# Kernel tuning notes

Measured on AMD Instinct MI355X. Metric: run time of the kernel, lower is better.

## Reference

```python
import jax, jax.numpy as jnp
import numpy as np

B, INPUTDIM, OUTDIM, GRIDSIZE = 4096, 128, 512, 300

def setup_inputs() -> dict:
    key = jax.random.key(0)
    k1, k2 = jax.random.split(key)
    x = jax.random.normal(k1, (B, INPUTDIM), dtype=jnp.float32)
    scale = 1.0 / (np.sqrt(INPUTDIM) * np.sqrt(GRIDSIZE))
    fouriercoeffs = jax.random.normal(k2, (2, OUTDIM, INPUTDIM, GRIDSIZE), dtype=jnp.float32) * scale
    return {"x": x, "fouriercoeffs": fouriercoeffs}

def reference(x, fouriercoeffs):
    # k: frequencies 1..gridsize
    gridsize = fouriercoeffs.shape[-1]
    k = jnp.arange(1, gridsize + 1, dtype=x.dtype)  # (G,)
    arg = x[:, :, None] * k  # (B, I, G)
    c = jnp.cos(arg)
    s = jnp.sin(arg)
    # einsum('dbik,djik->bj') with d=2 split into cos/sin terms
    y = jnp.einsum('big,jig->bj', c, fouriercoeffs[0]) + jnp.einsum('big,jig->bj', s, fouriercoeffs[1])
    return y
```

## Files before the change

### kernel.cpp

```cpp
#include <hip/hip_runtime.h>
#include <hip/hip_bf16.h>
#include <cstdint>

#define TB 256

typedef short short8 __attribute__((ext_vector_type(8)));
typedef float f32x4 __attribute__((ext_vector_type(4)));

constexpr int B_N = 4096, I_N = 128, J_N = 512, G_N = 300;
constexpr int K1 = I_N * G_N;
constexpr int BM = 128, BN = 256;
constexpr int NSP = 8;
constexpr int IC = 16;
constexpr float INV2PI = 0.15915494309189535f;

constexpr int GSTRIDE = 4 * 512 * 8;
constexpr size_t SPSTRIDE = (size_t)G_N * GSTRIDE;

__device__ __forceinline__ ushort f2bf(float f) {
    unsigned int u = __float_as_uint(f);
    return (ushort)((u + 0x7FFFu + ((u >> 16) & 1u)) >> 16);
}

__device__ __forceinline__ float fract_(float x) {
#if __has_builtin(__builtin_amdgcn_fractf)
    return __builtin_amdgcn_fractf(x);
#else
    return x - floorf(x);
#endif
}

__device__ __forceinline__ unsigned int pack_bf2(float a, float b) {
    __hip_bfloat162 h = __float22bfloat162_rn(make_float2(a, b));
    unsigned int u;
    __builtin_memcpy(&u, &h, 4);
    return u;
}

typedef __attribute__((address_space(3))) unsigned int lds_u32_t;
typedef __attribute__((address_space(1))) const unsigned int glb_u32_t;

__device__ __forceinline__ void llds16(const void* g, void* l) {
    __builtin_amdgcn_global_load_lds(
        reinterpret_cast<glb_u32_t*>(reinterpret_cast<uintptr_t>(g)),
        reinterpret_cast<lds_u32_t*>((unsigned int)reinterpret_cast<uintptr_t>(l)),
        16, 0, 0);
}

constexpr int TGC = 12;
__global__ __launch_bounds__(TB) void fkan_tr(const float* __restrict__ src,
                                              ushort* __restrict__ dst) {
    __shared__ __align__(16) ushort L[TGC * 2 * 32 * 8];
    const int bx = blockIdx.x;
    const int sp = bx & 7, djc = (bx >> 3) & 31, gc = bx >> 8;
    const int dj0 = djc * 32;
    const int d = dj0 >> 9;
    const int j0 = dj0 & 511;
    const int g0 = gc * TGC;
    const int tid = threadIdx.x;
    const int djl = tid >> 3, i2 = tid & 7;
    const int iA = sp * 16 + i2 * 2;
    const size_t rowA = ((size_t)(dj0 + djl) * 128 + iA) * 300;
    const int ihl = i2 >> 2;
    const int eA = (i2 & 3) * 2;

#pragma unroll
    for (int gq = 0; gq < TGC / 4; ++gq) {
        const int gg = g0 + gq * 4;
        float4 va = *(const float4*)(src + rowA + gg);
        float4 vb = *(const float4*)(src + rowA + 300 + gg);
        float a[4] = {va.x, va.y, va.z, va.w};
        float b[4] = {vb.x, vb.y, vb.z, vb.w};
#pragma unroll
        for (int t = 0; t < 4; ++t) {
            int gl = gq * 4 + t;
            unsigned int w = (unsigned int)f2bf(a[t]) | ((unsigned int)f2bf(b[t]) << 16);
            *(unsigned int*)&L[(((gl * 2 + ihl) * 32 + djl) * 8 + eA)] = w;
        }
    }
    __syncthreads();
    const uint4* Lv = (const uint4*)L;
#pragma unroll
    for (int it = 0; it < 3; ++it) {
        int s = it * 256 + tid;
        int gl = s >> 6, r = s & 63;
        int ih = r >> 5, jl = r & 31;
        size_t d16 = ((size_t)(sp * G_N + g0 + gl) * 4 + d * 2 + ih) * 512 + j0 + jl;
        ((uint4*)dst)[d16] = Lv[s];
    }
}

__global__ __launch_bounds__(TB, 2)
void fkan_gemm(const float* __restrict__ x,
               const ushort* __restrict__ fcb,
               float* __restrict__ out) {
    __shared__ __align__(16) ushort At[2 * 4 * 128 * 8];
    __shared__ __align__(16) ushort Bt[2 * 4 * 256 * 8];

    const int tid = threadIdx.x;
    const int bm = blockIdx.x, bn = blockIdx.y, sp = blockIdx.z;
    const int lane = tid & 63, wid = tid >> 6;
    const int wm = wid & 1, wn = wid >> 1;
    const int lhi = lane >> 4, llo = lane & 15;
    const int m = tid & 127, half = tid >> 7;

    float sv[8], cv[8], s0[8], c0[8];
    {
        const float* xr = x + ((size_t)(bm * BM + m)) * I_N + sp * IC + half * 8;
        float4 xa = *(const float4*)xr;
        float4 xb = *(const float4*)(xr + 4);
        float xv[8] = {xa.x, xa.y, xa.z, xa.w, xb.x, xb.y, xb.z, xb.w};
#pragma unroll
        for (int j = 0; j < 8; ++j) {
            float r = fract_(xv[j] * INV2PI);
            s0[j] = __builtin_amdgcn_sinf(r);
            c0[j] = __builtin_amdgcn_cosf(r);
            sv[j] = s0[j];
            cv[j] = c0[j];
        }
    }

    const ushort* bp[4];
#pragma unroll
    for (int q = 0; q < 4; ++q)
        bp[q] = fcb + (size_t)sp * SPSTRIDE
              + ((size_t)wid * 512 + bn * BN + q * 64 + lane) * 8;

    const int aoff = (lhi * 128 + wm * 64 + llo) * 8;
    const int boff = (lhi * 256 + wn * 128 + llo) * 8;
    ushort* awc0 = &At[(half * 128 + m) * 8];
    ushort* aws0 = &At[((2 + half) * 128 + m) * 8];

    f32x4 acc[4][8];
#pragma unroll
    for (int a = 0; a < 4; ++a)
#pragma unroll
        for (int b = 0; b < 8; ++b) acc[a][b] = (f32x4){0.f, 0.f, 0.f, 0.f};

    auto stageB = [&](int nb) {
#pragma unroll
        for (int q = 0; q < 4; ++q) {
            llds16(bp[q], (char*)Bt + (size_t)(nb * 1024 + wid * 256 + q * 64) * 16);
            bp[q] += GSTRIDE;
        }
    };
    auto writeA = [&](int nb) {
        uint4 vc = {pack_bf2(cv[0], cv[1]), pack_bf2(cv[2], cv[3]),
                    pack_bf2(cv[4], cv[5]), pack_bf2(cv[6], cv[7])};
        *(uint4*)(awc0 + nb * 4096) = vc;
        uint4 vs = {pack_bf2(sv[0], sv[1]), pack_bf2(sv[2], sv[3]),
                    pack_bf2(sv[4], sv[5]), pack_bf2(sv[6], sv[7])};
        *(uint4*)(aws0 + nb * 4096) = vs;
#pragma unroll
        for (int j = 0; j < 8; ++j) {
            float t = __builtin_fmaf(sv[j], c0[j], cv[j] * s0[j]);
            cv[j] = __builtin_fmaf(cv[j], c0[j], -(sv[j] * s0[j]));
            sv[j] = t;
        }
    };
    auto halfstep = [&](int cb, bool doNext) {
        __syncthreads();
        short8 af[4], bfr[8];
#pragma unroll
        for (int t = 0; t < 4; ++t)
            af[t] = *(const short8*)&At[cb * 4096 + aoff + t * 128];
#pragma unroll
        for (int t = 0; t < 8; ++t)
            bfr[t] = *(const short8*)&Bt[cb * 8192 + boff + t * 128];
        if (doNext) stageB(cb ^ 1);
#pragma unroll
        for (int tm = 0; tm < 4; ++tm)
#pragma unroll
            for (int tn = 0; tn < 8; ++tn)
                acc[tm][tn] = __builtin_amdgcn_mfma_f32_16x16x32_bf16(
                    af[tm], bfr[tn], acc[tm][tn], 0, 0, 0);
        if (doNext) writeA(cb ^ 1);
    };

    writeA(0);
    stageB(0);

    for (int g = 0; g < G_N; g += 2) {
        halfstep(0, true);
        halfstep(1, g + 2 < G_N);
    }

    const int row0 = bm * BM + wm * 64 + lhi * 4;
    const int col0 = bn * BN + wn * 128 + llo;
#pragma unroll
    for (int tm = 0; tm < 4; ++tm)
#pragma unroll
        for (int tn = 0; tn < 8; ++tn)
#pragma unroll
            for (int r = 0; r < 4; ++r)
                atomicAdd(&out[(size_t)(row0 + tm * 16 + r) * J_N + col0 + tn * 16],
                          acc[tm][tn][r]);
}

constexpr int SPL_FB = 4;
constexpr int KS_FB = 2 * K1 / SPL_FB;
constexpr int NSTEP_FB = KS_FB / 32;

__global__ __launch_bounds__(TB)
void fkan_gemm_fb(const float* __restrict__ x,
                  const float* __restrict__ fc32,
                  float* __restrict__ out) {
    __shared__ float xs[BM][65];
    __shared__ __align__(16) ushort At[4 * 128 * 8];
    __shared__ __align__(16) ushort Bt[4 * 128 * 8];

    const int tid = threadIdx.x;
    const int bm = blockIdx.x, bn = blockIdx.y, sp = blockIdx.z;
    const int d = sp >> 1;
    const int ib = (sp & 1) << 6;
    const int rbase = ib * G_N;

    for (int idx = tid; idx < BM * 64; idx += TB) {
        int row = idx >> 6, il = idx & 63;
        xs[row][il] = x[(size_t)(bm * BM + row) * I_N + ib + il];
    }

    f32x4 acc[4][4];
#pragma unroll
    for (int a = 0; a < 4; ++a)
#pragma unroll
        for (int b = 0; b < 4; ++b) acc[a][b] = (f32x4){0.f, 0.f, 0.f, 0.f};

    const int lane = tid & 63, wid = tid >> 6;
    const int wm = wid & 1, wn = wid >> 1;
    const int lhi = lane >> 4, llo = lane & 15;
    const int am = tid & 127, akg0 = tid >> 7;

    const float* f32base = fc32 + ((size_t)d * J_N + bn * 128) * K1 + rbase;

    for (int step = 0; step < NSTEP_FB; ++step) {
        __syncthreads();
#pragma unroll
        for (int it = 0; it < 2; ++it) {
            const int kg = akg0 + it * 2;
            int r = rbase + step * 32 + kg * 8;
            int i = (int)((unsigned)r / 300u);
            int g = r - i * 300;
            float xxv = xs[am][i - ib];
            float kkf = (float)(g + 1);
            short8 avv;
#pragma unroll
            for (int j = 0; j < 8; ++j) {
                float rev = xxv * kkf * INV2PI;
                float fr = fract_(rev) + (d ? 0.0f : 0.25f);
                avv[j] = (short)f2bf(__builtin_amdgcn_sinf(fract_(fr)));
                if (j < 7) {
                    ++g; kkf += 1.0f;
                    if (g == 300) { g = 0; kkf = 1.0f; ++i; xxv = xs[am][i - ib]; }
                }
            }
            *(short8*)&At[(kg * 128 + am) * 8] = avv;
        }
#pragma unroll
        for (int it = 0; it < 2; ++it) {
            int item = tid + it * TB;
            int n = item >> 2, grp = item & 3;
            const float* gp = f32base + (size_t)n * K1 + step * 32 + grp * 8;
            float4 v0 = *(const float4*)gp;
            float4 v1 = *(const float4*)(gp + 4);
            short8 bv;
            bv[0] = (short)f2bf(v0.x); bv[1] = (short)f2bf(v0.y);
            bv[2] = (short)f2bf(v0.z); bv[3] = (short)f2bf(v0.w);
            bv[4] = (short)f2bf(v1.x); bv[5] = (short)f2bf(v1.y);
            bv[6] = (short)f2bf(v1.z); bv[7] = (short)f2bf(v1.w);
            *(short8*)&Bt[(grp * 128 + n) * 8] = bv;
        }
        __syncthreads();
        short8 af[4], bf[4];
#pragma unroll
        for (int t = 0; t < 4; ++t) {
            af[t] = *(const short8*)&At[(lhi * 128 + wm * 64 + t * 16 + llo) * 8];
            bf[t] = *(const short8*)&Bt[(lhi * 128 + wn * 64 + t * 16 + llo) * 8];
        }
#pragma unroll
        for (int tm = 0; tm < 4; ++tm)
#pragma unroll
            for (int tn = 0; tn < 4; ++tn)
                acc[tm][tn] = __builtin_amdgcn_mfma_f32_16x16x32_bf16(
                    af[tm], bf[tn], acc[tm][tn], 0, 0, 0);
    }

    const int row0 = bm * BM + wm * 64 + lhi * 4;
    const int col0 = bn * 128 + wn * 64 + llo;
#pragma unroll
    for (int tm = 0; tm < 4; ++tm)
#pragma unroll
        for (int tn = 0; tn < 4; ++tn)
#pragma unroll
            for (int r = 0; r < 4; ++r)
                atomicAdd(&out[(size_t)(row0 + tm * 16 + r) * J_N + col0 + tn * 16],
                          acc[tm][tn][r]);
}

extern "C" void kernel_launch(void* const* d_in, const int* in_sizes, int n_in,
                              void* d_out, int out_size, void* d_ws, size_t ws_size,
                              hipStream_t stream) {
    const float* x = (const float*)d_in[0];
    const float* fc = (const float*)d_in[1];
    float* out = (float*)d_out;

    hipMemsetAsync(d_out, 0, (size_t)out_size * sizeof(float), stream);

    const size_t need = (size_t)2 * J_N * K1 * sizeof(ushort);

    if (ws_size >= need) {
        ushort* fcb = (ushort*)d_ws;
        fkan_tr<<<25 * 32 * 8, TB, 0, stream>>>(fc, fcb);
        dim3 grid(B_N / BM, J_N / BN, NSP);
        fkan_gemm<<<grid, TB, 0, stream>>>(x, fcb, out);
    } else {
        dim3 grid(B_N / BM, J_N / 128, SPL_FB);
        fkan_gemm_fb<<<grid, TB, 0, stream>>>(x, fc, out);
    }
}
```

Before: 551.9 us.

## Restructure weight transpose kernel with larger tiles, coalesced loads and LDS swizzle

The fp32-to-bf16 transpose kernel of the Fourier coefficients now processes 60 grid points per block with 512 threads. Each thread row reads 15 contiguous float4 chunks, so global loads are better coalesced. LDS writes and reads use an XOR swizzle to reduce bank conflicts. The trade-off is fewer, larger blocks with bigger LDS use, which may lower occupancy.

```diff
diff --git a/kernel.cpp b/kernel.cpp
--- a/kernel.cpp
+++ b/kernel.cpp
@@ -47,46 +47,51 @@
         16, 0, 0);
 }
 
-constexpr int TGC = 12;
-__global__ __launch_bounds__(TB) void fkan_tr(const float* __restrict__ src,
-                                              ushort* __restrict__ dst) {
-    __shared__ __align__(16) ushort L[TGC * 2 * 32 * 8];
-    const int bx = blockIdx.x;
-    const int sp = bx & 7, djc = (bx >> 3) & 31, gc = bx >> 8;
+constexpr int TRG = 60;
+constexpr int TRTB = 512;
+constexpr int TRUNITS = 256 * 15;
+
+__global__ __launch_bounds__(TRTB) void fkan_tr(const float* __restrict__ src,
+                                                ushort* __restrict__ dst) {
+    __shared__ __align__(16) ushort L[TRG * 2 * 32 * 8];
+    const int gc = blockIdx.x;
+    const int sp = blockIdx.y;
+    const int djc = blockIdx.z;
     const int dj0 = djc * 32;
     const int d = dj0 >> 9;
     const int j0 = dj0 & 511;
-    const int g0 = gc * TGC;
+    const int g0 = gc * TRG;
     const int tid = threadIdx.x;
-    const int djl = tid >> 3, i2 = tid & 7;
-    const int iA = sp * 16 + i2 * 2;
-    const size_t rowA = ((size_t)(dj0 + djl) * 128 + iA) * 300;
-    const int ihl = i2 >> 2;
-    const int eA = (i2 & 3) * 2;
-
-#pragma unroll
-    for (int gq = 0; gq < TGC / 4; ++gq) {
-        const int gg = g0 + gq * 4;
-        float4 va = *(const float4*)(src + rowA + gg);
-        float4 vb = *(const float4*)(src + rowA + 300 + gg);
+
+    unsigned int* Lw = (unsigned int*)L;
+
+    for (int u = tid; u < TRUNITS; u += TRTB) {
+        int rp = u / 15, c = u - rp * 15;
+        int djl = rp >> 3, ilp = rp & 7;
+        int ihl = ilp >> 2, e2 = ilp & 3;
+        const float* p = src + ((size_t)(dj0 + djl) * 128 + sp * 16 + ilp * 2) * 300
+                       + g0 + c * 4;
+        float4 va = *(const float4*)p;
+        float4 vb = *(const float4*)(p + 300);
         float a[4] = {va.x, va.y, va.z, va.w};
         float b[4] = {vb.x, vb.y, vb.z, vb.w};
-#pragma unroll
-        for (int t = 0; t < 4; ++t) {
-            int gl = gq * 4 + t;
-            unsigned int w = (unsigned int)f2bf(a[t]) | ((unsigned int)f2bf(b[t]) << 16);
-            *(unsigned int*)&L[(((gl * 2 + ihl) * 32 + djl) * 8 + eA)] = w;
+        const int swz = (c & 7) << 2;
+#pragma unroll
+        for (int k = 0; k < 4; ++k) {
+            int gl = c * 4 + k;
+            int wd = ((gl * 2 + ihl) * 32 + djl) * 4 + e2;
+            Lw[wd ^ swz] = pack_bf2(a[k], b[k]);
         }
     }
     __syncthreads();
+
     const uint4* Lv = (const uint4*)L;
-#pragma unroll
-    for (int it = 0; it < 3; ++it) {
-        int s = it * 256 + tid;
-        int gl = s >> 6, r = s & 63;
-        int ih = r >> 5, jl = r & 31;
-        size_t d16 = ((size_t)(sp * G_N + g0 + gl) * 4 + d * 2 + ih) * 512 + j0 + jl;
-        ((uint4*)dst)[d16] = Lv[s];
+    for (int w = tid; w < TRG * 64; w += TRTB) {
+        int gl = w >> 6, r = w & 63;
+        int ihl = r >> 5, jl = r & 31;
+        int q = (gl * 64 + ihl * 32 + jl) ^ ((gl >> 2) & 7);
+        size_t d16 = ((size_t)(sp * G_N + g0 + gl) * 4 + d * 2 + ihl) * 512 + j0 + jl;
+        ((uint4*)dst)[d16] = Lv[q];
     }
 }
 
@@ -310,7 +315,7 @@
 
     if (ws_size >= need) {
         ushort* fcb = (ushort*)d_ws;
-        fkan_tr<<<25 * 32 * 8, TB, 0, stream>>>(fc, fcb);
+        fkan_tr<<<dim3(5, 8, 32), TRTB, 0, stream>>>(fc, fcb);
         dim3 grid(B_N / BM, J_N / BN, NSP);
         fkan_gemm<<<grid, TB, 0, stream>>>(x, fcb, out);
     } else {
```

Result: faster. 535.2 us (-3.0%).
